# Performance work log

Hardware: AMD Instinct MI355X
Metric: run time of the kernel (lower is better)

## Reference

```python
import jax, jax.numpy as jnp
import numpy as np

B, S, H = 2, 2048, 4096
NH, NKV, HD = 32, 8, 128
EPS = 1e-6


def _rope_tables(seq_len, head_dim, base=10000.0):
    inv = 1.0 / (base ** (np.arange(0, head_dim, 2, dtype=np.float32) / head_dim))
    t = np.arange(seq_len, dtype=np.float32)
    freqs = np.outer(t, inv)                       # [S, HD/2]
    emb = np.concatenate([freqs, freqs], axis=-1)  # [S, HD] (HF rotate_half layout)
    return jnp.asarray(np.cos(emb)), jnp.asarray(np.sin(emb))


def setup_inputs() -> dict:
    key = jax.random.key(0)
    ks = jax.random.split(key, 6)
    x = jax.random.normal(ks[0], (B, S, H), dtype=jnp.float32)
    wq = jax.random.normal(ks[1], (NH * HD, H), dtype=jnp.float32) * 0.02
    wk = jax.random.normal(ks[2], (NKV * HD, H), dtype=jnp.float32) * 0.02
    wv = jax.random.normal(ks[3], (NKV * HD, H), dtype=jnp.float32) * 0.02
    wo = jax.random.normal(ks[4], (H, NH * HD), dtype=jnp.float32) * 0.02
    cos1, sin1 = _rope_tables(S, HD)
    cos = jnp.broadcast_to(cos1[None], (B, S, HD))
    sin = jnp.broadcast_to(sin1[None], (B, S, HD))
    return {
        "x": x, "cos": cos, "sin": sin,
        "wq": wq, "wk": wk, "wv": wv, "wo": wo,
        "q_norm_w": jnp.ones((HD,), jnp.float32),
        "k_norm_w": jnp.ones((HD,), jnp.float32),
    }


def _rms_norm(x, w):
    # fp32 RMSNorm over last dim, scaled by per-head-dim weight
    xf = x.astype(jnp.float32)
    n = xf * jax.lax.rsqrt(jnp.mean(xf * xf, axis=-1, keepdims=True) + EPS)
    return n.astype(x.dtype) * w


def _rotate_half(x):
    x1, x2 = jnp.split(x, 2, axis=-1)
    return jnp.concatenate([-x2, x1], axis=-1)


def reference(x, cos, sin, wq, wk, wv, wo, q_norm_w, k_norm_w):
    bs, seqlen, _ = x.shape
    # projections (nn.Linear: y = x @ W^T)
    xq = (x @ wq.T).reshape(bs, seqlen, NH, HD)
    xk = (x @ wk.T).reshape(bs, seqlen, NKV, HD)
    xv = (x @ wv.T).reshape(bs, seqlen, NKV, HD)
    # per-head RMSNorm before RoPE
    xq = _rms_norm(xq, q_norm_w)
    xk = _rms_norm(xk, k_norm_w)
    # [b, h, s, d]
    xq = xq.transpose(0, 2, 1, 3)
    xk = xk.transpose(0, 2, 1, 3)
    xv = xv.transpose(0, 2, 1, 3)
    # RoPE, cos/sin broadcast over heads
    c = cos[:, None, :, :]
    s = sin[:, None, :, :]
    xq = xq * c + _rotate_half(xq) * s
    xk = xk * c + _rotate_half(xk) * s
    # GQA: repeat kv heads
    rep = NH // NKV
    if rep > 1:
        xk = jnp.repeat(xk, rep, axis=1)
        xv = jnp.repeat(xv, rep, axis=1)
    # causal SDPA
    scale = 1.0 / jnp.sqrt(jnp.float32(HD))
    scores = jnp.einsum("bhqd,bhkd->bhqk", xq, xk) * scale
    mask = jnp.tril(jnp.ones((seqlen, seqlen), bool))
    scores = jnp.where(mask, scores, jnp.finfo(scores.dtype).min)
    probs = jax.nn.softmax(scores, axis=-1)
    out = jnp.einsum("bhqk,bhkd->bhqd", probs, xv)
    out = out.transpose(0, 2, 1, 3).reshape(bs, seqlen, NH * HD)
    return out @ wo.T
```

## Files before the change

### kernel.cpp

```cpp
#include <hip/hip_runtime.h>
#include <hip/hip_bf16.h>

#define NB  2
#define SS  2048
#define HH  4096
#define NH  32
#define NKV 8
#define HD  128
#define MR  (NB*SS)

typedef __bf16 bf16x8 __attribute__((ext_vector_type(8)));
typedef float  f32x4  __attribute__((ext_vector_type(4)));
typedef float  f32x16 __attribute__((ext_vector_type(16)));
using bf16 = __hip_bfloat16;

__device__ __forceinline__ f32x16 mfma32(bf16x8 a, bf16x8 b, f32x16 c) {
  return __builtin_amdgcn_mfma_f32_32x32x16_bf16(a, b, c, 0, 0, 0);
}
__device__ __forceinline__ unsigned cvtpk(float lo, float hi) {
  unsigned r; asm("v_cvt_pk_bf16_f32 %0, %1, %2" : "=v"(r) : "v"(lo), "v"(hi));
  return r;
}
__device__ __forceinline__ void swap32(unsigned &a, unsigned &b) {
  asm volatile("v_permlane32_swap_b32 %0, %1" : "+v"(a), "+v"(b));
}
__device__ __forceinline__ float fexp2(float x) {
  float r; asm("v_exp_f32 %0, %1" : "=v"(r) : "v"(x)); return r;
}

typedef const __attribute__((address_space(1))) void gv_t;
typedef __attribute__((address_space(3))) void lv_t;
__device__ __forceinline__ void gload16(const void* g, void* l) {
  __builtin_amdgcn_global_load_lds((gv_t*)g, (lv_t*)l, 16, 0, 0);
}
#define CFENCE asm volatile("" ::: "memory")

__global__ void f2b(const float* __restrict__ s, bf16* __restrict__ d, int n)
{
  int i = blockIdx.x*blockDim.x + threadIdx.x;
  int stride = gridDim.x*blockDim.x;
  for (int idx = i*4; idx < n; idx += stride*4) {
    float4 v = *(const float4*)(s + idx);
    __hip_bfloat16 b0 = __float2bfloat16(v.x);
    __hip_bfloat16 b1 = __float2bfloat16(v.y);
    __hip_bfloat16 b2 = __float2bfloat16(v.z);
    __hip_bfloat16 b3 = __float2bfloat16(v.w);
    ushort4 o;
    o.x = *reinterpret_cast<unsigned short*>(&b0);
    o.y = *reinterpret_cast<unsigned short*>(&b1);
    o.z = *reinterpret_cast<unsigned short*>(&b2);
    o.w = *reinterpret_cast<unsigned short*>(&b3);
    *(ushort4*)((unsigned short*)d + idx) = o;
  }
}

template<typename OutT>
__global__ __launch_bounds__(512, 2) void gemm256(
    const bf16* __restrict__ A, const bf16* __restrict__ Bt, OutT* __restrict__ C,
    int M, int N, int K, int tilesX)
{
  __shared__ bf16 lds[2*2*2*16384/2];

  const int bid = blockIdx.x;
  const int cpx = gridDim.x >> 3;
  const int wg  = (bid & 7)*cpx + (bid >> 3);
  const int m0 = (wg / tilesX) * 256, n0 = (wg % tilesX) * 256;

  const int tid = threadIdx.x;
  const int l = tid & 63;
  const int l31 = l & 31, hi = (l >> 5) & 1;
  const int wid = tid >> 6;
  const int wr = wid >> 2, wc = wid & 3;

  const int srow = tid >> 2;
  const int sps  = tid & 3;
  const int sls  = (sps - (srow >> 1)) & 3;
  const bf16* ga0 = A  + (size_t)(m0 + srow)*K       + sls*8;
  const bf16* ga1 = A  + (size_t)(m0 + srow + 128)*K + sls*8;
  const bf16* gb0 = Bt + (size_t)(n0 + srow)*K       + sls*8;
  const bf16* gb1 = Bt + (size_t)(n0 + srow + 128)*K + sls*8;
  const int ldst = tid*8;

#define REG(buf, ab, ks) (&lds[(((buf)*2 + (ab))*2 + (ks))*8192])
#define STG(buf, ks, kofs) do {                                   \
    gload16(ga0 + (kofs), REG(buf,0,ks) + ldst);                  \
    gload16(ga1 + (kofs), REG(buf,0,ks) + ldst + 4096);           \
    gload16(gb0 + (kofs), REG(buf,1,ks) + ldst);                  \
    gload16(gb1 + (kofs), REG(buf,1,ks) + ldst + 4096);           \
  } while (0)

  f32x16 acc[4][2];
  #pragma unroll
  for (int fm = 0; fm < 4; ++fm)
    #pragma unroll
    for (int fn = 0; fn < 2; ++fn)
      #pragma unroll
      for (int e = 0; e < 16; ++e) acc[fm][fn][e] = 0.f;

  const int arow = wr*128 + l31;
  const int brow = wc*64  + l31;
  const int rot  = (l31 >> 1) & 3;
  const int ps0  = ((0 + hi) + rot) & 3;
  const int ps1  = ((2 + hi) + rot) & 3;

  const int nt = K >> 6;
  STG(0, 0, 0); STG(0, 1, 32);
  asm volatile("s_waitcnt vmcnt(4)" ::: "memory");
  __builtin_amdgcn_s_barrier();
  CFENCE;

  for (int t = 0; t < nt; ++t) {
    const int p = t & 1, nb = p ^ 1;
    const bool pf = (t + 1) < nt;
    const int kn = (t + 1) << 6;
    #pragma unroll
    for (int s = 0; s < 2; ++s) {
      if (pf) {
        if (s == 0) STG(nb, 0, kn);
        else        STG(nb, 1, kn + 32);
      }
      const bf16* Ar = REG(p, 0, s);
      const bf16* Br = REG(p, 1, s);
      bf16x8 af[4][2], bv[2][2];
      #pragma unroll
      for (int fm = 0; fm < 4; ++fm) {
        af[fm][0] = *(const bf16x8*)(Ar + (arow + fm*32)*32 + ps0*8);
        af[fm][1] = *(const bf16x8*)(Ar + (arow + fm*32)*32 + ps1*8);
      }
      #pragma unroll
      for (int fn = 0; fn < 2; ++fn) {
        bv[fn][0] = *(const bf16x8*)(Br + (brow + fn*32)*32 + ps0*8);
        bv[fn][1] = *(const bf16x8*)(Br + (brow + fn*32)*32 + ps1*8);
      }
      __builtin_amdgcn_s_setprio(1);
      #pragma unroll
      for (int st = 0; st < 2; ++st)
        #pragma unroll
        for (int fm = 0; fm < 4; ++fm)
          #pragma unroll
          for (int fn = 0; fn < 2; ++fn)
            acc[fm][fn] = mfma32(af[fm][st], bv[fn][st], acc[fm][fn]);
      __builtin_amdgcn_s_setprio(0);
      if (pf || s == 0) asm volatile("s_waitcnt vmcnt(4)" ::: "memory");
      else              asm volatile("s_waitcnt vmcnt(0)" ::: "memory");
      __builtin_amdgcn_s_barrier();
      CFENCE;
    }
  }
#undef STG
#undef REG

  #pragma unroll
  for (int fm = 0; fm < 4; ++fm) {
    #pragma unroll
    for (int fn = 0; fn < 2; ++fn) {
      const int ccol = n0 + wc*64 + fn*32 + l31;
      #pragma unroll
      for (int r = 0; r < 16; ++r) {
        const int crow = m0 + wr*128 + fm*32 + (r & 3) + 8*(r >> 2) + 4*hi;
        if constexpr (sizeof(OutT) == 2)
          C[(size_t)crow*N + ccol] = __float2bfloat16(acc[fm][fn][r]);
        else
          C[(size_t)crow*N + ccol] = acc[fm][fn][r];
      }
    }
  }
}

__global__ __launch_bounds__(256) void normrope(
    const bf16* __restrict__ src, bf16* __restrict__ dst,
    const float* __restrict__ cosb, const float* __restrict__ sinb,
    const float* __restrict__ w, int nh, float scale, int rowstride, int coloff)
{
  const int wid = threadIdx.x >> 6, lane = threadIdx.x & 63;
  const int row = blockIdx.x*4 + wid;
  const int m = row / nh, h = row % nh;
  const int b = m / SS, s = m % SS;
  const bf16* sp = src + (size_t)m*rowstride + coloff + h*HD;
  float v1 = __bfloat162float(sp[lane]);
  float v2 = __bfloat162float(sp[lane + 64]);
  float ss = v1*v1 + v2*v2;
  #pragma unroll
  for (int msk = 1; msk < 64; msk <<= 1) ss += __shfl_xor(ss, msk);
  float r = rsqrtf(ss*(1.f/128.f) + 1e-6f) * scale;
  float n1 = v1*r*w[lane], n2 = v2*r*w[lane + 64];
  const float* cp  = cosb + (size_t)m*HD;
  const float* sip = sinb + (size_t)m*HD;
  float o1 = n1*cp[lane]      - n2*sip[lane];
  float o2 = n2*cp[lane + 64] + n1*sip[lane + 64];
  bf16* dp = dst + ((size_t)(b*nh + h)*SS + s)*HD;
  dp[lane]      = __float2bfloat16(o1);
  dp[lane + 64] = __float2bfloat16(o2);
}

__global__ __launch_bounds__(256) void vtrans(const bf16* __restrict__ v0,
                                              bf16* __restrict__ vt,
                                              int rowstride, int coloff)
{
  __shared__ bf16 tile[64][65];
  const int s0 = blockIdx.x*64, d0 = blockIdx.y*64, bkv = blockIdx.z;
  const int bb = bkv >> 3, kv = bkv & 7;
  const int c = threadIdx.x & 63, rbase = threadIdx.x >> 6;
  #pragma unroll
  for (int r = 0; r < 64; r += 4) {
    int sl = r + rbase;
    tile[sl][c] = v0[(size_t)(bb*SS + s0 + sl)*rowstride + coloff + kv*HD + d0 + c];
  }
  __syncthreads();
  #pragma unroll
  for (int r = 0; r < 64; r += 4) {
    int dl = r + rbase;
    vt[((size_t)bkv*HD + d0 + dl)*SS + s0 + c] = tile[c][dl];
  }
}

__global__ __launch_bounds__(512, 2) void attn_fwd(
    const bf16* __restrict__ qr, const bf16* __restrict__ kr,
    const bf16* __restrict__ vt, bf16* __restrict__ ao)
{
  __shared__ __align__(16) char smem[65536];

  const int L = blockIdx.x;
  const int orig = (L & 7)*64 + (L >> 3);
  const int bh = orig >> 3, j = orig & 7;
  const int b = bh >> 5, h = bh & 31, kvh = h >> 2;

  const int tid = threadIdx.x;
  const int wid = tid >> 6, lane = tid & 63;
  const int l31 = lane & 31, hi = lane >> 5;
  const unsigned hi16 = hi << 4;
  const unsigned swz = (lane & 7) << 4;

  const int qw0 = (wid < 4) ? (j*128 + wid*32) : ((15 - j)*128 + (wid - 4)*32);
  const int NT = 32 - 2*j;
  const int qlane = qw0 + l31;

  const bf16* Qp = qr + ((size_t)(b*NH + h)*SS + qlane)*HD;
  const bf16* Kp = kr + (size_t)(b*NKV + kvh)*SS*HD;
  const bf16* Vp = vt + (size_t)(b*NKV + kvh)*HD*SS;

  const int krA = tid >> 4;
  const int ksA = tid & 15;
  const int vrA = tid >> 3;
  const int vsA = tid & 7;
  const int kswz = (ksA ^ (krA & 7))*8;
  const int vswz = (vsA ^ (vrA & 7))*8;

#define STAGE_ATTN(buf, kvbase) do {                                        \
    char* kb = smem + (buf)*32768;                                          \
    char* vb = kb + 16384;                                                  \
    gload16(Kp + (size_t)(krA + (kvbase))*HD + kswz,      kb + tid*16);     \
    gload16(Kp + (size_t)(krA + 32 + (kvbase))*HD + kswz, kb + 8192 + tid*16); \
    gload16(Vp + (size_t)vrA*SS + (kvbase) + vswz,        vb + tid*16);     \
    gload16(Vp + (size_t)(vrA + 64)*SS + (kvbase) + vswz, vb + 8192 + tid*16); \
  } while (0)

  STAGE_ATTN(0, 0);
  bf16x8 qf[8];
  #pragma unroll
  for (int kd = 0; kd < 8; ++kd)
    qf[kd] = *(const bf16x8*)(Qp + kd*16 + hi*8);
  asm volatile("s_waitcnt vmcnt(0)" ::: "memory");
  __builtin_amdgcn_s_barrier();
  CFENCE;

  f32x16 o0, o1, o2, o3;
  #pragma unroll
  for (int r = 0; r < 16; ++r) { o0[r] = 0.f; o1[r] = 0.f; o2[r] = 0.f; o3[r] = 0.f; }
  float mrow = -1e30f, lrow = 0.f;

  for (int t = 0; t < NT; ++t) {
    const int p = t & 1;
    const char* KsB = smem + p*32768;
    const char* VsB = KsB + 16384;
    if (t + 1 < NT) STAGE_ATTN(p ^ 1, (t + 1)*64);
    const int kv0 = t*64;

    if (kv0 <= qw0 + 31) {
      f32x16 s0, s1;
      #pragma unroll
      for (int r = 0; r < 16; ++r) { s0[r] = 0.f; s1[r] = 0.f; }
      #pragma unroll
      for (int kd = 0; kd < 8; ++kd) {
        bf16x8 k0f = *(const bf16x8*)(KsB + l31*256        + (((unsigned)(kd*32) + hi16) ^ swz));
        bf16x8 k1f = *(const bf16x8*)(KsB + (32 + l31)*256 + (((unsigned)(kd*32) + hi16) ^ swz));
        s0 = mfma32(k0f, qf[kd], s0);
        s1 = mfma32(k1f, qf[kd], s1);
      }
      if (kv0 + 63 > qw0) {
        #pragma unroll
        for (int r = 0; r < 16; ++r) {
          const int off = (r & 3) + 8*(r >> 2) + 4*hi;
          if (kv0 + off > qlane)      s0[r] = -1e30f;
          if (kv0 + 32 + off > qlane) s1[r] = -1e30f;
        }
      }
      float tmax = s0[0];
      #pragma unroll
      for (int r = 1; r < 16; ++r) tmax = fmaxf(tmax, s0[r]);
      #pragma unroll
      for (int r = 0; r < 16; ++r) tmax = fmaxf(tmax, s1[r]);
      tmax = fmaxf(tmax, __shfl_xor(tmax, 32));
      if (!__all(tmax <= mrow + 8.f)) {
        float mnew = fmaxf(mrow, tmax);
        float alpha = fexp2(mrow - mnew);
        mrow = mnew;
        lrow *= alpha;
        #pragma unroll
        for (int r = 0; r < 16; ++r) {
          o0[r] *= alpha; o1[r] *= alpha; o2[r] *= alpha; o3[r] *= alpha;
        }
      }
      float tsum = 0.f;
      #pragma unroll
      for (int r = 0; r < 16; ++r) { s0[r] = fexp2(s0[r] - mrow); tsum += s0[r]; }
      #pragma unroll
      for (int r = 0; r < 16; ++r) { s1[r] = fexp2(s1[r] - mrow); tsum += s1[r]; }
      tsum += __shfl_xor(tsum, 32);
      lrow += tsum;

      #pragma unroll
      for (int ks = 0; ks < 4; ++ks) {
        const int bb0 = (ks & 1)*8;
        float p0,p1,p2,p3,p4,p5,p6,p7;
        if (ks < 2) { p0=s0[bb0+0];p1=s0[bb0+1];p2=s0[bb0+2];p3=s0[bb0+3];
                      p4=s0[bb0+4];p5=s0[bb0+5];p6=s0[bb0+6];p7=s0[bb0+7]; }
        else        { p0=s1[bb0+0];p1=s1[bb0+1];p2=s1[bb0+2];p3=s1[bb0+3];
                      p4=s1[bb0+4];p5=s1[bb0+5];p6=s1[bb0+6];p7=s1[bb0+7]; }
        unsigned c01 = cvtpk(p0,p1), c23 = cvtpk(p2,p3);
        unsigned c45 = cvtpk(p4,p5), c67 = cvtpk(p6,p7);
        unsigned w0 = c01, w2 = c45; swap32(w0, w2);
        unsigned w1 = c23, w3 = c67; swap32(w1, w3);
        union { unsigned u[4]; bf16x8 v; } pa;
        pa.u[0]=w0; pa.u[1]=w1; pa.u[2]=w2; pa.u[3]=w3;
        #pragma unroll
        for (int dt = 0; dt < 4; ++dt) {
          bf16x8 vf = *(const bf16x8*)(VsB + (dt*32 + l31)*128 +
                                       (((unsigned)(ks*32) + hi16) ^ swz));
          f32x16 &oo = (dt==0)?o0:(dt==1)?o1:(dt==2)?o2:o3;
          oo = mfma32(vf, pa.v, oo);
        }
      }
    }

    asm volatile("s_waitcnt vmcnt(0)" ::: "memory");
    __builtin_amdgcn_s_barrier();
    CFENCE;
  }
#undef STAGE_ATTN

  const float invl = 1.f / lrow;
  char* ow = smem + wid*4096;
  bf16* aop = ao + ((size_t)b*SS + qlane)*HH + h*HD;
  const unsigned eswz = (l31 & 7) << 4;
  #pragma unroll
  for (int half = 0; half < 2; ++half) {
    #pragma unroll
    for (int hh = 0; hh < 2; ++hh) {
      #pragma unroll
      for (int r = 0; r < 16; ++r) {
        const int dcol = hh*32 + (r & 3) + 8*(r >> 2) + 4*hi;
        float val = ((half*2+hh)==0 ? o0[r] : (half*2+hh)==1 ? o1[r]
                     : (half*2+hh)==2 ? o2[r] : o3[r]) * invl;
        *(bf16*)(ow + l31*128 + (((unsigned)(dcol*2)) ^ eswz)) = __float2bfloat16(val);
      }
    }
    #pragma unroll
    for (int m = 0; m < 4; ++m) {
      const int c0 = hi*32 + m*8;
      bf16x8 vv = *(const bf16x8*)(ow + l31*128 + (((unsigned)(c0*2)) ^ eswz));
      *(bf16x8*)(aop + half*64 + c0) = vv;
    }
  }
}

extern "C" void kernel_launch(void* const* d_in, const int* in_sizes, int n_in,
                              void* d_out, int out_size, void* d_ws, size_t ws_size,
                              hipStream_t stream)
{
  const float* x    = (const float*)d_in[0];
  const float* cosb = (const float*)d_in[1];
  const float* sinb = (const float*)d_in[2];
  const float* wq   = (const float*)d_in[3];
  const float* wk   = (const float*)d_in[4];
  const float* wv   = (const float*)d_in[5];
  const float* wo   = (const float*)d_in[6];
  const float* qnw  = (const float*)d_in[7];
  const float* knw  = (const float*)d_in[8];
  float* out = (float*)d_out;

  char* ws = (char*)d_ws;
  bf16* xb    = (bf16*)(ws);
  bf16* wqkvb = (bf16*)(ws +  33554432);
  bf16* wob   = (bf16*)(ws +  83886080);
  bf16* qkv0  = (bf16*)(ws + 117440512);
  bf16* qr    = (bf16*)(ws + 167772160);
  bf16* vt = xb;
  bf16* kr = (bf16*)(ws + 8388608);
  bf16* ao = qkv0;

  f2b<<<2048, 256, 0, stream>>>(x,  xb,  MR*HH);
  f2b<<<2048, 256, 0, stream>>>(wq, wqkvb,                      NH*HD*HH);
  f2b<<<2048, 256, 0, stream>>>(wk, wqkvb + (size_t)4096*4096, NKV*HD*HH);
  f2b<<<2048, 256, 0, stream>>>(wv, wqkvb + (size_t)5120*4096, NKV*HD*HH);
  f2b<<<2048, 256, 0, stream>>>(wo, wob, HH*NH*HD);

  gemm256<bf16><<<384, 512, 0, stream>>>(xb, wqkvb, qkv0, MR, 6144, HH, 24);

  normrope<<<(MR*NH)/4,  256, 0, stream>>>(qkv0, qr, cosb, sinb, qnw, NH,
                                           0.08838834764831845f*1.44269504088896341f,
                                           6144, 0);
  normrope<<<(MR*NKV)/4, 256, 0, stream>>>(qkv0, kr, cosb, sinb, knw, NKV, 1.0f,
                                           6144, 4096);
  vtrans<<<dim3(32, 2, 16), 256, 0, stream>>>(qkv0, vt, 6144, 5120);

  attn_fwd<<<512, 512, 0, stream>>>(qr, kr, vt, ao);

  gemm256<float><<<256, 512, 0, stream>>>(ao, wob, out, MR, HH, HH, 16);
}
```

Baseline: 595.6 us.

## Switch GEMM to 16x16x32 MFMA with finer-grained interleaved load/compute phases

```diff
diff --git a/kernel.cpp b/kernel.cpp
--- a/kernel.cpp
+++ b/kernel.cpp
@@ -14,6 +14,9 @@
 typedef float  f32x16 __attribute__((ext_vector_type(16)));
 using bf16 = __hip_bfloat16;
 
+__device__ __forceinline__ f32x4 mfma16(bf16x8 a, bf16x8 b, f32x4 c) {
+  return __builtin_amdgcn_mfma_f32_16x16x32_bf16(a, b, c, 0, 0, 0);
+}
 __device__ __forceinline__ f32x16 mfma32(bf16x8 a, bf16x8 b, f32x16 c) {
   return __builtin_amdgcn_mfma_f32_32x32x16_bf16(a, b, c, 0, 0, 0);
 }
@@ -59,7 +62,7 @@
     const bf16* __restrict__ A, const bf16* __restrict__ Bt, OutT* __restrict__ C,
     int M, int N, int K, int tilesX)
 {
-  __shared__ bf16 lds[2*2*2*16384/2];
+  __shared__ bf16 lds[2*2*2*8192];
 
   const int bid = blockIdx.x;
   const int cpx = gridDim.x >> 3;
@@ -68,7 +71,7 @@
 
   const int tid = threadIdx.x;
   const int l = tid & 63;
-  const int l31 = l & 31, hi = (l >> 5) & 1;
+  const int l15 = l & 15, lhi = l >> 4;
   const int wid = tid >> 6;
   const int wr = wid >> 2, wc = wid & 3;
 
@@ -81,87 +84,104 @@
   const bf16* gb1 = Bt + (size_t)(n0 + srow + 128)*K + sls*8;
   const int ldst = tid*8;
 
-#define REG(buf, ab, ks) (&lds[(((buf)*2 + (ab))*2 + (ks))*8192])
-#define STG(buf, ks, kofs) do {                                   \
+#define REG(buf, mat, ks) (&lds[(((buf)*2 + (mat))*2 + (ks))*8192])
+#define STG_A(buf, ks, kofs) do {                                 \
     gload16(ga0 + (kofs), REG(buf,0,ks) + ldst);                  \
     gload16(ga1 + (kofs), REG(buf,0,ks) + ldst + 4096);           \
+  } while (0)
+#define STG_B(buf, ks, kofs) do {                                 \
     gload16(gb0 + (kofs), REG(buf,1,ks) + ldst);                  \
     gload16(gb1 + (kofs), REG(buf,1,ks) + ldst + 4096);           \
   } while (0)
 
-  f32x16 acc[4][2];
-  #pragma unroll
-  for (int fm = 0; fm < 4; ++fm)
+  f32x4 acc[8][4];
+  #pragma unroll
+  for (int fm = 0; fm < 8; ++fm)
     #pragma unroll
-    for (int fn = 0; fn < 2; ++fn)
-      #pragma unroll
-      for (int e = 0; e < 16; ++e) acc[fm][fn][e] = 0.f;
-
-  const int arow = wr*128 + l31;
-  const int brow = wc*64  + l31;
-  const int rot  = (l31 >> 1) & 3;
-  const int ps0  = ((0 + hi) + rot) & 3;
-  const int ps1  = ((2 + hi) + rot) & 3;
+    for (int fn = 0; fn < 4; ++fn)
+      #pragma unroll
+      for (int e = 0; e < 4; ++e) acc[fm][fn][e] = 0.f;
+
+  const int arow = wr*128 + l15;
+  const int brow = wc*64  + l15;
+  const int psl  = (lhi + (l15 >> 1)) & 3;
+
+  bf16x8 bv[4];
+
+#define PHASE(PB, KS, FMH, RB, STG, WN) do {                               \
+    const bf16* Ar_ = REG(PB, 0, KS);                                      \
+    const bf16* Br_ = REG(PB, 1, KS);                                      \
+    bf16x8 af[4];                                                          \
+    for (int fm = 0; fm < 4; ++fm)                                         \
+      af[fm] = *(const bf16x8*)(Ar_ + (arow + (FMH)*64 + fm*16)*32 + psl*8); \
+    if (RB) {                                                              \
+      for (int fn = 0; fn < 4; ++fn)                                       \
+        bv[fn] = *(const bf16x8*)(Br_ + (brow + fn*16)*32 + psl*8);        \
+    }                                                                      \
+    STG;                                                                   \
+    CFENCE;                                                                \
+    __builtin_amdgcn_s_barrier();                                          \
+    __builtin_amdgcn_s_setprio(1);                                         \
+    for (int fm = 0; fm < 4; ++fm)                                         \
+      for (int fn = 0; fn < 4; ++fn)                                       \
+        acc[(FMH)*4 + fm][fn] = mfma16(af[fm], bv[fn], acc[(FMH)*4 + fm][fn]); \
+    __builtin_amdgcn_s_setprio(0);                                         \
+    if ((WN) == 4)      asm volatile("s_waitcnt vmcnt(4)" ::: "memory");   \
+    else if ((WN) == 0) asm volatile("s_waitcnt vmcnt(0)" ::: "memory");   \
+    __builtin_amdgcn_s_barrier();                                          \
+    CFENCE;                                                                \
+  } while (0)
 
   const int nt = K >> 6;
-  STG(0, 0, 0); STG(0, 1, 32);
-  asm volatile("s_waitcnt vmcnt(4)" ::: "memory");
+
+  STG_A(0, 0, 0);  STG_B(0, 0, 0);  STG_A(0, 1, 32);  STG_B(0, 1, 32);
+  STG_A(1, 0, 64); STG_B(1, 0, 64); STG_B(1, 1, 96);
+  asm volatile("s_waitcnt vmcnt(6)" ::: "memory");
   __builtin_amdgcn_s_barrier();
   CFENCE;
 
-  for (int t = 0; t < nt; ++t) {
-    const int p = t & 1, nb = p ^ 1;
-    const bool pf = (t + 1) < nt;
-    const int kn = (t + 1) << 6;
+  for (int i = 0; i < (nt >> 1) - 1; ++i) {
+    const int t  = i << 1;
+    const int k1 = ((t + 1) << 6) + 32;
+    const int k2 = (t + 2) << 6;
+    const int k3 = (t + 3) << 6;
+    PHASE(0, 0, 0, true,  STG_A(1, 1, k1),      -1);
+    PHASE(0, 0, 1, false, STG_B(0, 0, k2),      -1);
+    PHASE(0, 1, 0, true,  STG_A(0, 0, k2),      -1);
+    PHASE(0, 1, 1, false, STG_B(0, 1, k2 + 32),  4);
+    PHASE(1, 0, 0, true,  STG_A(0, 1, k2 + 32), -1);
+    PHASE(1, 0, 1, false, STG_B(1, 0, k3),      -1);
+    PHASE(1, 1, 0, true,  STG_A(1, 0, k3),      -1);
+    PHASE(1, 1, 1, false, STG_B(1, 1, k3 + 32),  4);
+  }
+  {
+    const int k1 = ((nt - 1) << 6) + 32;
+    PHASE(0, 0, 0, true,  STG_A(1, 1, k1), -1);
+    PHASE(0, 0, 1, false, (void)0,         -1);
+    PHASE(0, 1, 0, true,  (void)0,         -1);
+    PHASE(0, 1, 1, false, (void)0,          0);
+    PHASE(1, 0, 0, true,  (void)0,         -1);
+    PHASE(1, 0, 1, false, (void)0,         -1);
+    PHASE(1, 1, 0, true,  (void)0,         -1);
+    PHASE(1, 1, 1, false, (void)0,         -1);
+  }
+#undef PHASE
+#undef STG_A
+#undef STG_B
+#undef REG
+
+  #pragma unroll
+  for (int fm = 0; fm < 8; ++fm) {
+    const int crow = m0 + wr*128 + fm*16 + lhi*4;
     #pragma unroll
-    for (int s = 0; s < 2; ++s) {
-      if (pf) {
-        if (s == 0) STG(nb, 0, kn);
-        else        STG(nb, 1, kn + 32);
-      }
-      const bf16* Ar = REG(p, 0, s);
-      const bf16* Br = REG(p, 1, s);
-      bf16x8 af[4][2], bv[2][2];
-      #pragma unroll
-      for (int fm = 0; fm < 4; ++fm) {
-        af[fm][0] = *(const bf16x8*)(Ar + (arow + fm*32)*32 + ps0*8);
-        af[fm][1] = *(const bf16x8*)(Ar + (arow + fm*32)*32 + ps1*8);
-      }
-      #pragma unroll
-      for (int fn = 0; fn < 2; ++fn) {
-        bv[fn][0] = *(const bf16x8*)(Br + (brow + fn*32)*32 + ps0*8);
-        bv[fn][1] = *(const bf16x8*)(Br + (brow + fn*32)*32 + ps1*8);
-      }
-      __builtin_amdgcn_s_setprio(1);
-      #pragma unroll
-      for (int st = 0; st < 2; ++st)
-        #pragma unroll
-        for (int fm = 0; fm < 4; ++fm)
-          #pragma unroll
-          for (int fn = 0; fn < 2; ++fn)
-            acc[fm][fn] = mfma32(af[fm][st], bv[fn][st], acc[fm][fn]);
-      __builtin_amdgcn_s_setprio(0);
-      if (pf || s == 0) asm volatile("s_waitcnt vmcnt(4)" ::: "memory");
-      else              asm volatile("s_waitcnt vmcnt(0)" ::: "memory");
-      __builtin_amdgcn_s_barrier();
-      CFENCE;
-    }
-  }
-#undef STG
-#undef REG
-
-  #pragma unroll
-  for (int fm = 0; fm < 4; ++fm) {
-    #pragma unroll
-    for (int fn = 0; fn < 2; ++fn) {
-      const int ccol = n0 + wc*64 + fn*32 + l31;
-      #pragma unroll
-      for (int r = 0; r < 16; ++r) {
-        const int crow = m0 + wr*128 + fm*32 + (r & 3) + 8*(r >> 2) + 4*hi;
+    for (int fn = 0; fn < 4; ++fn) {
+      const int ccol = n0 + wc*64 + fn*16 + l15;
+      #pragma unroll
+      for (int j = 0; j < 4; ++j) {
         if constexpr (sizeof(OutT) == 2)
-          C[(size_t)crow*N + ccol] = __float2bfloat16(acc[fm][fn][r]);
+          C[(size_t)(crow + j)*N + ccol] = __float2bfloat16(acc[fm][fn][j]);
         else
-          C[(size_t)crow*N + ccol] = acc[fm][fn][r];
+          C[(size_t)(crow + j)*N + ccol] = acc[fm][fn][j];
       }
     }
   }
```

New measurement: 544.6 us. 8.6% less time.
